# Optimization experiments

Measured on AMD Instinct MI355X. Metric: run time of the kernel, lower is better.

The kernel has to match this reference:

```python
import jax, jax.numpy as jnp
import numpy as np

N = 100_000      # num nodes
R = 7            # num relations
D = 64           # input_dim == output_dim
E = 1_600_000    # num edges
EDIM = 16        # edge_input_dim


def setup_inputs() -> dict:
    key = jax.random.key(0)
    ks = jax.random.split(key, 10)
    node_in = jax.random.randint(ks[0], (E,), 0, N)
    node_out = jax.random.randint(ks[1], (E,), 0, N)
    relation = jax.random.randint(ks[2], (E,), 0, R)
    edge_list = jnp.stack([node_in, node_out, relation], axis=1)  # (E, 3)
    x = jax.random.normal(ks[3], (N, D), dtype=jnp.float32)
    edge_weight = jax.random.uniform(ks[4], (E,), dtype=jnp.float32)
    edge_feature = jax.random.normal(ks[5], (E, EDIM), dtype=jnp.float32)
    s = 1.0 / np.sqrt(R * D)
    W_lin = jax.random.uniform(ks[6], (D, R * D), minval=-s, maxval=s, dtype=jnp.float32)
    b_lin = jnp.zeros((D,), jnp.float32)
    s2 = 1.0 / np.sqrt(D)
    W_self = jax.random.uniform(ks[7], (D, D), minval=-s2, maxval=s2, dtype=jnp.float32)
    b_self = jnp.zeros((D,), jnp.float32)
    s3 = 1.0 / np.sqrt(EDIM)
    W_edge = jax.random.uniform(ks[8], (D, EDIM), minval=-s3, maxval=s3, dtype=jnp.float32)
    b_edge = jnp.zeros((D,), jnp.float32)
    return {"x": x, "edge_list": edge_list, "edge_weight": edge_weight,
            "edge_feature": edge_feature, "W_lin": W_lin, "b_lin": b_lin,
            "W_self": W_self, "b_self": b_self, "W_edge": W_edge, "b_edge": b_edge}


def reference(x, edge_list, edge_weight, edge_feature, W_lin, b_lin, W_self, b_self, W_edge, b_edge):
    node_in, node_out, relation = edge_list[:, 0], edge_list[:, 1], edge_list[:, 2]
    # destination index in the flattened (node, relation) space
    seg = node_out * R + relation  # (E,)
    # sparse.mm(adj.T, x): scatter w * x[src] into (N*R, D)
    msg = edge_weight[:, None] * x[node_in]  # (E, D)
    update = jax.ops.segment_sum(msg, seg, num_segments=N * R)  # (N*R, D)
    # edge feature branch: edge_linear then weighted scatter_add
    edge_msg = (edge_feature @ W_edge.T + b_edge) * edge_weight[:, None]  # (E, D)
    update = update + jax.ops.segment_sum(edge_msg, seg, num_segments=N * R)
    update = update.reshape(N, R * D)
    out = update @ W_lin.T + b_lin + x @ W_self.T + b_self
    return jax.nn.relu(out)
```

## Files before the change

### kernel.cpp

```cpp
#include <hip/hip_runtime.h>
#include <hip/hip_bf16.h>
#include <hip/hip_fp16.h>

#define N_NODES 100000
#define R_REL   7
#define E_EDGES 1600000
#define EDIM    16
#define KTOT    640
#define KSTR    648
#define CAP     56
#define CSTR    16

typedef __bf16 bf16_t;
typedef bf16_t bf16x8 __attribute__((ext_vector_type(8)));
typedef bf16_t bf16x4 __attribute__((ext_vector_type(4)));
typedef float  f32x4  __attribute__((ext_vector_type(4)));
typedef unsigned long long u64;

#define RFL(v) __builtin_amdgcn_readfirstlane(v)
#define RL(v, l) __builtin_amdgcn_readlane(v, l)


__device__ __forceinline__ void sc1(int e, int src, int dst, int rel, float w,
                                    int* __restrict__ cnt, u64* __restrict__ recs8) {
    unsigned wb = __float_as_uint(w) & 0xFFFFFE00u;
    int slot = atomicAdd(&cnt[dst * CSTR], 1);
    unsigned u0 = (unsigned)src | ((unsigned)rel << 17) | ((unsigned)(e & 0xFFF) << 20);
    unsigned u1 = ((unsigned)e >> 12) | wb;
    recs8[(size_t)dst * CAP + slot] = ((u64)u1 << 32) | u0;
}

__global__ __launch_bounds__(256) void k_pre(
    const float* __restrict__ x, const int* __restrict__ el,
    const float* __restrict__ wgt,
    const float* __restrict__ W_lin, const float* __restrict__ W_self,
    const float* __restrict__ W_edge, const float* __restrict__ b_edge,
    int* __restrict__ cnt, bf16_t* __restrict__ xb, bf16_t* __restrict__ Bp,
    u64* __restrict__ recs8)
{
    const int t = blockIdx.x * 256 + threadIdx.x;

    if (t < (N_NODES * 64) / 16) {
        const float4* xp = (const float4*)(x + (size_t)t * 16);
        float4 v0 = xp[0], v1 = xp[1], v2 = xp[2], v3 = xp[3];
        bf16x8 o0 = {(bf16_t)v0.x, (bf16_t)v0.y, (bf16_t)v0.z, (bf16_t)v0.w,
                     (bf16_t)v1.x, (bf16_t)v1.y, (bf16_t)v1.z, (bf16_t)v1.w};
        bf16x8 o1 = {(bf16_t)v2.x, (bf16_t)v2.y, (bf16_t)v2.z, (bf16_t)v2.w,
                     (bf16_t)v3.x, (bf16_t)v3.y, (bf16_t)v3.z, (bf16_t)v3.w};
        *(bf16x8*)(xb + (size_t)t * 16)     = o0;
        *(bf16x8*)(xb + (size_t)t * 16 + 8) = o1;
    }

    if (t < KTOT * 64) {
        int k = t >> 6;
        int j = t & 63;
        float v;
        if (k < 448) {
            v = W_lin[j * 448 + k];
        } else if (k < 512) {
            v = W_self[j * 64 + (k - 448)];
        } else if (k < 624) {
            int r = (k - 512) >> 4, kk = (k - 512) & 15;
            float sacc = 0.f;
            for (int d = 0; d < 64; d++)
                sacc = fmaf(W_lin[j * 448 + r * 64 + d], W_edge[d * 16 + kk], sacc);
            v = sacc;
        } else if (k < 631) {
            int r = k - 624;
            float sacc = 0.f;
            for (int d = 0; d < 64; d++)
                sacc = fmaf(W_lin[j * 448 + r * 64 + d], b_edge[d], sacc);
            v = sacc;
        } else {
            v = 0.f;
        }
        Bp[((k >> 3) * 64 + j) * 8 + (k & 7)] = (bf16_t)v;
    }

    if (t < E_EDGES / 4) {
        const int4* ep = (const int4*)(el + (size_t)t * 12);
        int4 q0 = ep[0], q1 = ep[1], q2 = ep[2];
        float4 w4 = *(const float4*)(wgt + (size_t)t * 4);
        int e = t * 4;
        sc1(e + 0, q0.x, q0.y, q0.z, w4.x, cnt, recs8);
        sc1(e + 1, q0.w, q1.x, q1.y, w4.y, cnt, recs8);
        sc1(e + 2, q1.z, q1.w, q2.x, w4.z, cnt, recs8);
        sc1(e + 3, q2.y, q2.z, q2.w, w4.w, cnt, recs8);
    }
}


__global__ __launch_bounds__(256) void k_main(
    const bf16_t* __restrict__ xb, const float* __restrict__ ef,
    const float* __restrict__ b_lin, const float* __restrict__ b_self,
    const int* __restrict__ cnt, const u64* __restrict__ recs8,
    const bf16_t* __restrict__ Bp, float* __restrict__ out)
{
    __shared__ __align__(16) bf16_t A[16 * KSTR];
    const int wave = threadIdx.x >> 6;
    const int lane = threadIdx.x & 63;
    const int lef  = lane & 15;
    const int nodeBase = blockIdx.x * 16;
    const int n0 = nodeBase + wave * 4;

    int    md[4];
    u64    rw[4];
    bf16_t sv[4];
#pragma unroll
    for (int i = 0; i < 4; i++) {
        md[i] = cnt[(n0 + i) * CSTR];
        rw[i] = recs8[(size_t)(n0 + i) * CAP + min(lane, CAP - 1)];
        sv[i] = xb[(n0 + i) * 64 + lane];
    }

#pragma unroll
    for (int i = 0; i < 4; i++) {
        const int row = wave * 4 + i;
        bf16_t* Ar = A + row * KSTR;
        Ar[448 + lane] = sv[i];
        if (lane < 9) Ar[631 + lane] = (bf16_t)0.f;

        int m = min(md[i], CAP);
        const unsigned u0v = (unsigned)rw[i];
        const unsigned u1v = (unsigned)(rw[i] >> 32);
        const int  relv  = (u0v >> 17) & 7;
        const bool valid = lane < m;

        for (int r = 0; r < R_REL; r++) {
            u64 mr = __ballot(valid && (relv == r));
            float a = 0.f, F = 0.f, s = 0.f;
            while (mr) {
                int i0 = __builtin_ctzll(mr); mr &= mr - 1;
                int i1 = i0; bool two = false, more = false;
                if (mr) { i1 = __builtin_ctzll(mr); mr &= mr - 1;
                          two = true; more = (mr != 0); }
                unsigned a0 = RL(u0v, i0), b0 = RL(u1v, i0);
                unsigned a1 = RL(u0v, i1), b1 = RL(u1v, i1);
                int src0 = a0 & 0x1FFFF, src1 = a1 & 0x1FFFF;
                int e0 = (a0 >> 20) | ((b0 & 0x1FF) << 12);
                int e1 = (a1 >> 20) | ((b1 & 0x1FF) << 12);
                float w0 = __uint_as_float(b0 & 0xFFFFFE00u);
                float w1 = two ? __uint_as_float(b1 & 0xFFFFFE00u) : 0.f;
                float xv0 = (float)xb[src0 * 64 + lane];
                float xv1 = (float)xb[src1 * 64 + lane];
                float ev0 = ef[e0 * EDIM + lef];
                float ev1 = ef[e1 * EDIM + lef];
                if (more) {
                    int i2 = __builtin_ctzll(mr); mr &= mr - 1;
                    int i3 = i2; bool four = false;
                    if (mr) { i3 = __builtin_ctzll(mr); mr &= mr - 1; four = true; }
                    unsigned a2 = RL(u0v, i2), b2 = RL(u1v, i2);
                    unsigned a3 = RL(u0v, i3), b3 = RL(u1v, i3);
                    int src2 = a2 & 0x1FFFF, src3 = a3 & 0x1FFFF;
                    int e2 = (a2 >> 20) | ((b2 & 0x1FF) << 12);
                    int e3 = (a3 >> 20) | ((b3 & 0x1FF) << 12);
                    float w2 = __uint_as_float(b2 & 0xFFFFFE00u);
                    float w3 = four ? __uint_as_float(b3 & 0xFFFFFE00u) : 0.f;
                    float xv2 = (float)xb[src2 * 64 + lane];
                    float xv3 = (float)xb[src3 * 64 + lane];
                    float ev2 = ef[e2 * EDIM + lef];
                    float ev3 = ef[e3 * EDIM + lef];
                    a = fmaf(w2, xv2, a); F = fmaf(w2, ev2, F); s += w2;
                    a = fmaf(w3, xv3, a); F = fmaf(w3, ev3, F); s += w3;
                }
                a = fmaf(w0, xv0, a); F = fmaf(w0, ev0, F); s += w0;
                a = fmaf(w1, xv1, a); F = fmaf(w1, ev1, F); s += w1;
            }
            Ar[r * 64 + lane] = (bf16_t)a;
            if (lane < EDIM) Ar[512 + r * EDIM + lane] = (bf16_t)F;
            if (lane == 0)   Ar[624 + r] = (bf16_t)s;
        }
    }
    __syncthreads();

    const int quad = lane >> 4;
    const int l15  = lane & 15;
    f32x4 c = {0.f, 0.f, 0.f, 0.f};
#pragma unroll
    for (int s2i = 0; s2i < KTOT / 32; s2i++) {
        bf16x8 a = *(const bf16x8*)(A + l15 * KSTR + s2i * 32 + quad * 8);
        bf16x8 b = *(const bf16x8*)(Bp + (((s2i * 4 + quad) * 64) + wave * 16 + l15) * 8);
        c = __builtin_amdgcn_mfma_f32_16x16x32_bf16(a, b, c, 0, 0, 0);
    }
    const int j = wave * 16 + l15;
    const float bias = b_lin[j] + b_self[j];
#pragma unroll
    for (int q = 0; q < 4; q++) {
        const int n = nodeBase + quad * 4 + q;
        float v = c[q] + bias;
        out[n * 64 + j] = v > 0.f ? v : 0.f;
    }
}


extern "C" void kernel_launch(void* const* d_in, const int* in_sizes, int n_in,
                              void* d_out, int out_size, void* d_ws, size_t ws_size,
                              hipStream_t stream) {
    const float* x      = (const float*)d_in[0];
    const int*   el     = (const int*)  d_in[1];
    const float* wgt    = (const float*)d_in[2];
    const float* ef     = (const float*)d_in[3];
    const float* W_lin  = (const float*)d_in[4];
    const float* b_lin  = (const float*)d_in[5];
    const float* W_self = (const float*)d_in[6];
    const float* b_self = (const float*)d_in[7];
    const float* W_edge = (const float*)d_in[8];
    const float* b_edge = (const float*)d_in[9];
    float* out = (float*)d_out;

    u64*    recs8 = (u64*)d_ws;
    int*    cnt   = (int*)(recs8 + (size_t)N_NODES * CAP);
    bf16_t* xb    = (bf16_t*)(cnt + (size_t)N_NODES * CSTR);
    bf16_t* Bp    = xb + (size_t)N_NODES * 64;

    hipMemsetAsync(cnt, 0, (size_t)N_NODES * CSTR * sizeof(int), stream);
    k_pre <<<1563, 256, 0, stream>>>(x, el, wgt, W_lin, W_self, W_edge, b_edge,
                                     cnt, xb, Bp, recs8);
    k_main<<<N_NODES / 16, 256, 0, stream>>>(xb, ef, b_lin, b_self,
                                             cnt, recs8, Bp, out);
}
```

Measured before the change: 378.3 us.

## Swizzle shared A tile, batch edge atomics, tighten gather loop, raise occupancy

Replaces the padded shared-memory row stride with an XOR-swizzled 1280-byte row layout to avoid LDS bank conflicts on MFMA operand reads. The edge bucketing in k_pre now issues all four atomics before the record stores, which lets their latencies overlap. k_main sets a launch-bounds occupancy hint of 8, masks record loads beyond the count, and restructures the per-relation gather loop so single edges no longer waste a duplicate load. The occupancy hint may cause register pressure or spills.

After: 380.9 us. Within noise of the previous version (+0.7%).

```diff
diff --git a/kernel.cpp b/kernel.cpp
--- a/kernel.cpp
+++ b/kernel.cpp
@@ -7,9 +7,11 @@
 #define E_EDGES 1600000
 #define EDIM    16
 #define KTOT    640
-#define KSTR    648
+#define AROWB   1280
 #define CAP     56
 #define CSTR    16
+
+#define ASWZ(row, cb) ((row) * AROWB + ((cb) ^ (((row) & 7) << 4)))
 
 typedef __bf16 bf16_t;
 typedef bf16_t bf16x8 __attribute__((ext_vector_type(8)));
@@ -20,15 +22,6 @@
 #define RFL(v) __builtin_amdgcn_readfirstlane(v)
 #define RL(v, l) __builtin_amdgcn_readlane(v, l)
 
-
-__device__ __forceinline__ void sc1(int e, int src, int dst, int rel, float w,
-                                    int* __restrict__ cnt, u64* __restrict__ recs8) {
-    unsigned wb = __float_as_uint(w) & 0xFFFFFE00u;
-    int slot = atomicAdd(&cnt[dst * CSTR], 1);
-    unsigned u0 = (unsigned)src | ((unsigned)rel << 17) | ((unsigned)(e & 0xFFF) << 20);
-    unsigned u1 = ((unsigned)e >> 12) | wb;
-    recs8[(size_t)dst * CAP + slot] = ((u64)u1 << 32) | u0;
-}
 
 __global__ __launch_bounds__(256) void k_pre(
     const float* __restrict__ x, const int* __restrict__ el,
@@ -81,22 +74,34 @@
         const int4* ep = (const int4*)(el + (size_t)t * 12);
         int4 q0 = ep[0], q1 = ep[1], q2 = ep[2];
         float4 w4 = *(const float4*)(wgt + (size_t)t * 4);
-        int e = t * 4;
-        sc1(e + 0, q0.x, q0.y, q0.z, w4.x, cnt, recs8);
-        sc1(e + 1, q0.w, q1.x, q1.y, w4.y, cnt, recs8);
-        sc1(e + 2, q1.z, q1.w, q2.x, w4.z, cnt, recs8);
-        sc1(e + 3, q2.y, q2.z, q2.w, w4.w, cnt, recs8);
+        const int e = t * 4;
+        const int srcs[4] = {q0.x, q0.w, q1.z, q2.y};
+        const int dsts[4] = {q0.y, q1.x, q1.w, q2.z};
+        const int rels[4] = {q0.z, q1.y, q2.x, q2.w};
+        const float ws[4] = {w4.x, w4.y, w4.z, w4.w};
+        int slot[4];
+#pragma unroll
+        for (int i = 0; i < 4; i++)
+            slot[i] = atomicAdd(&cnt[dsts[i] * CSTR], 1);
+#pragma unroll
+        for (int i = 0; i < 4; i++) {
+            unsigned u0 = (unsigned)srcs[i] | ((unsigned)rels[i] << 17)
+                        | ((unsigned)((e + i) & 0xFFF) << 20);
+            unsigned u1 = ((unsigned)(e + i) >> 12)
+                        | (__float_as_uint(ws[i]) & 0xFFFFFE00u);
+            recs8[(size_t)dsts[i] * CAP + slot[i]] = ((u64)u1 << 32) | u0;
+        }
     }
 }
 
 
-__global__ __launch_bounds__(256) void k_main(
+__global__ __launch_bounds__(256, 8) void k_main(
     const bf16_t* __restrict__ xb, const float* __restrict__ ef,
     const float* __restrict__ b_lin, const float* __restrict__ b_self,
     const int* __restrict__ cnt, const u64* __restrict__ recs8,
     const bf16_t* __restrict__ Bp, float* __restrict__ out)
 {
-    __shared__ __align__(16) bf16_t A[16 * KSTR];
+    __shared__ __align__(16) unsigned char A[16 * AROWB];
     const int wave = threadIdx.x >> 6;
     const int lane = threadIdx.x & 63;
     const int lef  = lane & 15;
@@ -108,19 +113,18 @@
     bf16_t sv[4];
 #pragma unroll
     for (int i = 0; i < 4; i++) {
-        md[i] = cnt[(n0 + i) * CSTR];
-        rw[i] = recs8[(size_t)(n0 + i) * CAP + min(lane, CAP - 1)];
+        md[i] = min(cnt[(n0 + i) * CSTR], CAP);
+        rw[i] = (lane < md[i]) ? recs8[(size_t)(n0 + i) * CAP + lane] : 0ull;
         sv[i] = xb[(n0 + i) * 64 + lane];
     }
 
 #pragma unroll
     for (int i = 0; i < 4; i++) {
         const int row = wave * 4 + i;
-        bf16_t* Ar = A + row * KSTR;
-        Ar[448 + lane] = sv[i];
-        if (lane < 9) Ar[631 + lane] = (bf16_t)0.f;
-
-        int m = min(md[i], CAP);
+        *(bf16_t*)(A + ASWZ(row, (448 + lane) * 2)) = sv[i];
+        if (lane < 9) *(bf16_t*)(A + ASWZ(row, (631 + lane) * 2)) = (bf16_t)0.f;
+
+        const int m = md[i];
         const unsigned u0v = (unsigned)rw[i];
         const unsigned u1v = (unsigned)(rw[i] >> 32);
         const int  relv  = (u0v >> 17) & 7;
@@ -131,54 +135,60 @@
             float a = 0.f, F = 0.f, s = 0.f;
             while (mr) {
                 int i0 = __builtin_ctzll(mr); mr &= mr - 1;
-                int i1 = i0; bool two = false, more = false;
-                if (mr) { i1 = __builtin_ctzll(mr); mr &= mr - 1;
-                          two = true; more = (mr != 0); }
                 unsigned a0 = RL(u0v, i0), b0 = RL(u1v, i0);
-                unsigned a1 = RL(u0v, i1), b1 = RL(u1v, i1);
-                int src0 = a0 & 0x1FFFF, src1 = a1 & 0x1FFFF;
+                int src0 = a0 & 0x1FFFF;
                 int e0 = (a0 >> 20) | ((b0 & 0x1FF) << 12);
-                int e1 = (a1 >> 20) | ((b1 & 0x1FF) << 12);
                 float w0 = __uint_as_float(b0 & 0xFFFFFE00u);
-                float w1 = two ? __uint_as_float(b1 & 0xFFFFFE00u) : 0.f;
                 float xv0 = (float)xb[src0 * 64 + lane];
-                float xv1 = (float)xb[src1 * 64 + lane];
                 float ev0 = ef[e0 * EDIM + lef];
-                float ev1 = ef[e1 * EDIM + lef];
-                if (more) {
-                    int i2 = __builtin_ctzll(mr); mr &= mr - 1;
-                    int i3 = i2; bool four = false;
-                    if (mr) { i3 = __builtin_ctzll(mr); mr &= mr - 1; four = true; }
-                    unsigned a2 = RL(u0v, i2), b2 = RL(u1v, i2);
-                    unsigned a3 = RL(u0v, i3), b3 = RL(u1v, i3);
-                    int src2 = a2 & 0x1FFFF, src3 = a3 & 0x1FFFF;
-                    int e2 = (a2 >> 20) | ((b2 & 0x1FF) << 12);
-                    int e3 = (a3 >> 20) | ((b3 & 0x1FF) << 12);
-                    float w2 = __uint_as_float(b2 & 0xFFFFFE00u);
-                    float w3 = four ? __uint_as_float(b3 & 0xFFFFFE00u) : 0.f;
-                    float xv2 = (float)xb[src2 * 64 + lane];
-                    float xv3 = (float)xb[src3 * 64 + lane];
-                    float ev2 = ef[e2 * EDIM + lef];
-                    float ev3 = ef[e3 * EDIM + lef];
-                    a = fmaf(w2, xv2, a); F = fmaf(w2, ev2, F); s += w2;
-                    a = fmaf(w3, xv3, a); F = fmaf(w3, ev3, F); s += w3;
+                if (mr) {
+                    int i1 = __builtin_ctzll(mr); mr &= mr - 1;
+                    unsigned a1 = RL(u0v, i1), b1 = RL(u1v, i1);
+                    int src1 = a1 & 0x1FFFF;
+                    int e1 = (a1 >> 20) | ((b1 & 0x1FF) << 12);
+                    float w1 = __uint_as_float(b1 & 0xFFFFFE00u);
+                    float xv1 = (float)xb[src1 * 64 + lane];
+                    float ev1 = ef[e1 * EDIM + lef];
+                    if (mr) {
+                        int i2 = __builtin_ctzll(mr); mr &= mr - 1;
+                        int i3 = i2; bool four = false;
+                        if (mr) { i3 = __builtin_ctzll(mr); mr &= mr - 1; four = true; }
+                        unsigned a2 = RL(u0v, i2), b2 = RL(u1v, i2);
+                        unsigned a3 = RL(u0v, i3), b3 = RL(u1v, i3);
+                        int src2 = a2 & 0x1FFFF, src3 = a3 & 0x1FFFF;
+                        int e2 = (a2 >> 20) | ((b2 & 0x1FF) << 12);
+                        int e3 = (a3 >> 20) | ((b3 & 0x1FF) << 12);
+                        float w2 = __uint_as_float(b2 & 0xFFFFFE00u);
+                        float w3 = four ? __uint_as_float(b3 & 0xFFFFFE00u) : 0.f;
+                        float xv2 = (float)xb[src2 * 64 + lane];
+                        float xv3 = (float)xb[src3 * 64 + lane];
+                        float ev2 = ef[e2 * EDIM + lef];
+                        float ev3 = ef[e3 * EDIM + lef];
+                        a = fmaf(w2, xv2, a); F = fmaf(w2, ev2, F); s += w2;
+                        a = fmaf(w3, xv3, a); F = fmaf(w3, ev3, F); s += w3;
+                    }
+                    a = fmaf(w1, xv1, a); F = fmaf(w1, ev1, F); s += w1;
                 }
                 a = fmaf(w0, xv0, a); F = fmaf(w0, ev0, F); s += w0;
-                a = fmaf(w1, xv1, a); F = fmaf(w1, ev1, F); s += w1;
             }
-            Ar[r * 64 + lane] = (bf16_t)a;
-            if (lane < EDIM) Ar[512 + r * EDIM + lane] = (bf16_t)F;
-            if (lane == 0)   Ar[624 + r] = (bf16_t)s;
+            *(bf16_t*)(A + ASWZ(row, (r * 64 + lane) * 2)) = (bf16_t)a;
+            if (lane < EDIM)
+                *(bf16_t*)(A + ASWZ(row, (512 + r * EDIM + lane) * 2)) = (bf16_t)F;
+            if (lane == 0)
+                *(bf16_t*)(A + ASWZ(row, (624 + r) * 2)) = (bf16_t)s;
         }
     }
     __syncthreads();
 
     const int quad = lane >> 4;
     const int l15  = lane & 15;
+    const unsigned abase = (unsigned)l15 * AROWB;
+    const unsigned aswz  = (unsigned)((l15 & 7) << 4);
     f32x4 c = {0.f, 0.f, 0.f, 0.f};
 #pragma unroll
     for (int s2i = 0; s2i < KTOT / 32; s2i++) {
-        bf16x8 a = *(const bf16x8*)(A + l15 * KSTR + s2i * 32 + quad * 8);
+        bf16x8 a = *(const bf16x8*)(A + abase
+                     + (((unsigned)(s2i * 64 + quad * 16)) ^ aswz));
         bf16x8 b = *(const bf16x8*)(Bp + (((s2i * 4 + quad) * 64) + wave * 16 + l15) * 8);
         c = __builtin_amdgcn_mfma_f32_16x16x32_bf16(a, b, c, 0, 0, 0);
     }
```
